# Performance work log

Hardware: AMD Instinct MI355X
Metric: run time of the kernel (lower is better)

The kernel has to match this reference:

```python
import jax, jax.numpy as jnp
import numpy as np

N_NODES = 100000

def gcn_conv(x, edge_index, W, b):
    # torch_geometric GCNConv: add self-loops, sym-normalize, aggregate, add bias
    n = x.shape[0]
    loop = jnp.arange(n)
    src = jnp.concatenate([edge_index[0], loop])  # [E+N]
    dst = jnp.concatenate([edge_index[1], loop])
    h = x @ W  # [N, out]
    deg = jax.ops.segment_sum(jnp.ones_like(dst, dtype=h.dtype), dst, num_segments=n)
    dinv = jnp.where(deg > 0, jax.lax.rsqrt(deg), 0.0)
    norm = dinv[src] * dinv[dst]  # [E+N]
    msg = h[src] * norm[:, None]  # gather + scale
    out = jax.ops.segment_sum(msg, dst, num_segments=n)  # scatter-add
    return out + b

def setup_inputs() -> dict:
    key = jax.random.key(0)
    ks = jax.random.split(key, 6)
    N, F, H, C, E = N_NODES, 128, 128, 32, 1600000
    x = jax.random.normal(ks[0], (N, F), dtype=jnp.float32)
    edge_index = jax.random.randint(ks[1], (2, E), 0, N, dtype=jnp.int64)
    W1 = jax.random.normal(ks[2], (F, H), dtype=jnp.float32) * (1.0 / np.sqrt(F))
    b1 = jnp.zeros((H,), jnp.float32)
    W2 = jax.random.normal(ks[3], (H, H), dtype=jnp.float32) * (1.0 / np.sqrt(H))
    b2 = jnp.zeros((H,), jnp.float32)
    Wc = jax.random.normal(ks[4], (H, C), dtype=jnp.float32) * (1.0 / np.sqrt(H))
    bc = jnp.zeros((C,), jnp.float32)
    return {"x": x, "edge_index": edge_index, "W1": W1, "b1": b1, "W2": W2, "b2": b2, "Wc": Wc, "bc": bc}

def reference(x, edge_index, W1, b1, W2, b2, Wc, bc):
    h = jax.nn.relu(gcn_conv(x, edge_index, W1, b1))
    # dropout is identity in eval mode
    h = jax.nn.relu(gcn_conv(h, edge_index, W2, b2))
    pooled = jnp.mean(h, axis=0)  # [H]
    return pooled @ Wc + bc  # [C]
```

## Files before the change

kernel.cpp:

```cpp
#include <hip/hip_runtime.h>
#include <hip/hip_bf16.h>


#define FEAT 128
#define CHUNK 4096
#define MAXBUCK 512
#define ECAP 12288
#define PBLK 512
#define BPAD 3856

typedef __attribute__((ext_vector_type(8))) short short8;
typedef __attribute__((ext_vector_type(4))) float float4v;
typedef __attribute__((ext_vector_type(2))) float floatx2;

union I4S8 { int4 i; short8 s; };

static __device__ inline unsigned short f2bf(float f) {
    union { __hip_bfloat16 h; unsigned short u; } cv;
    cv.h = __float2bfloat16(f);
    return cv.u;
}

static __device__ inline floatx2 fp8x2_dec(unsigned int u) {
#if __has_builtin(__builtin_amdgcn_cvt_pk_f32_fp8)
    return __builtin_amdgcn_cvt_pk_f32_fp8((int)u, false);
#else
    floatx2 r;
    unsigned int b0 = u & 0xFFu, b1 = (u >> 8) & 0xFFu;
    r.x = __uint_as_float(((b0 & 0x80u) << 24) | ((b0 & 0x7Fu) << 20)) * 0x1p+120f;
    r.y = __uint_as_float(((b1 & 0x80u) << 24) | ((b1 & 0x7Fu) << 20)) * 0x1p+120f;
    return r;
#endif
}

static __device__ inline floatx2 fp8x2_dec_hi(unsigned int u) {
#if __has_builtin(__builtin_amdgcn_cvt_pk_f32_fp8)
    return __builtin_amdgcn_cvt_pk_f32_fp8((int)u, true);
#else
    return fp8x2_dec(u >> 16);
#endif
}

static __device__ inline unsigned short fp8x2_enc(float x, float y) {
#if __has_builtin(__builtin_amdgcn_cvt_pk_fp8_f32)
    return (unsigned short)(__builtin_amdgcn_cvt_pk_fp8_f32(x, y, 0, false) & 0xFFFF);
#else
    auto enc1 = [](float f) -> unsigned int {
        unsigned int u = __float_as_uint(f);
        unsigned int s = (u >> 24) & 0x80u;
        float a = fabsf(f);
        a = fminf(a, 448.0f);
        unsigned int code;
        if (a < 0.015625f) {
            code = (unsigned int)(int)rintf(a * 512.0f);
        } else {
            unsigned int au = __float_as_uint(a);
            unsigned int r = au + 0x0007FFFFu + ((au >> 20) & 1u);
            unsigned int e = (r >> 23) - 120u;
            unsigned int m = (r >> 20) & 7u;
            code = (e << 3) | m;
            if (code > 0x7Eu) code = 0x7Eu;
        }
        return code | s;
    };
    return (unsigned short)(enc1(x) | (enc1(y) << 8));
#endif
}

static __device__ inline unsigned char fp8enc(float f) {
#if __has_builtin(__builtin_amdgcn_cvt_pk_fp8_f32)
    return (unsigned char)(__builtin_amdgcn_cvt_pk_fp8_f32(f, 0.0f, 0, false) & 0xFF);
#else
    return (unsigned char)(fp8x2_enc(f, 0.0f) & 0xFF);
#endif
}

__global__ __launch_bounds__(256) void hist2(const int* __restrict__ dst,
                                             int* __restrict__ hist,
                                             int nE, int NC, int nbuck) {
    __shared__ int h[MAXBUCK];
    int c = blockIdx.x, t = threadIdx.x;
    for (int i = t; i < nbuck; i += 256) h[i] = 0;
    __syncthreads();
    int beg = c * CHUNK, end = min(nE, beg + CHUNK);
    for (int e = beg + t; e < end; e += 256)
        atomicAdd(&h[dst[e] >> 8], 1);
    __syncthreads();
    for (int i = t; i < nbuck; i += 256) hist[i * NC + c] = h[i];
}

__global__ __launch_bounds__(256) void rowsum_k(const int* __restrict__ hist,
                                                int* __restrict__ btot, int NC) {
    __shared__ int red[256];
    int b = blockIdx.x, t = threadIdx.x;
    int s = 0;
    for (int c = t; c < NC; c += 256) s += hist[b * NC + c];
    red[t] = s;
    __syncthreads();
    for (int o = 128; o > 0; o >>= 1) {
        if (t < o) red[t] += red[t + o];
        __syncthreads();
    }
    if (t == 0) btot[b] = red[0];
}

__global__ __launch_bounds__(512) void bscan_k(const int* __restrict__ btot,
                                               int* __restrict__ bboff, int nbuck) {
    __shared__ int sc[512];
    int t = threadIdx.x;
    int v = (t < nbuck) ? btot[t] : 0;
    sc[t] = v;
    __syncthreads();
    for (int o = 1; o < 512; o <<= 1) {
        int add = (t >= o) ? sc[t - o] : 0;
        __syncthreads();
        sc[t] += add;
        __syncthreads();
    }
    if (t < nbuck) {
        bboff[t] = sc[t] - v;
        if (t == nbuck - 1) bboff[nbuck] = sc[t];
    }
}

__global__ __launch_bounds__(512) void rowoff_k(const int* __restrict__ hist,
                                                const int* __restrict__ bboff,
                                                int* __restrict__ hoff, int NC) {
    __shared__ int sc[512];
    int b = blockIdx.x, t = threadIdx.x;
    int v = (t < NC) ? hist[b * NC + t] : 0;
    sc[t] = v;
    __syncthreads();
    for (int o = 1; o < 512; o <<= 1) {
        int add = (t >= o) ? sc[t - o] : 0;
        __syncthreads();
        sc[t] += add;
        __syncthreads();
    }
    if (t < NC) hoff[b * NC + t] = bboff[b] + sc[t] - v;
}

__global__ __launch_bounds__(256) void fill2(const int* __restrict__ src,
                                             const int* __restrict__ dst,
                                             const int* __restrict__ off,
                                             int* __restrict__ binned,
                                             int nE, int NC, int nbuck) {
    __shared__ int cur[MAXBUCK];
    int c = blockIdx.x, t = threadIdx.x;
    for (int i = t; i < nbuck; i += 256) cur[i] = off[i * NC + c];
    __syncthreads();
    int beg = c * CHUNK, end = min(nE, beg + CHUNK);
    for (int e = beg + t; e < end; e += 256) {
        int d = dst[e];
        int pos = atomicAdd(&cur[d >> 8], 1);
        binned[pos] = (src[e] << 8) | (d & 255);
    }
}

__global__ __launch_bounds__(256) void bucket_scat(const int* __restrict__ binned,
                                                   const int* __restrict__ bboff,
                                                   int* __restrict__ cnt,
                                                   float* __restrict__ dinv,
                                                   int* __restrict__ cursor,
                                                   int* __restrict__ csr_src, int n) {
    __shared__ int se[ECAP];
    __shared__ int lcnt[256];
    __shared__ int lcur[256];
    __shared__ int ssc[256];
    int b = blockIdx.x, t = threadIdx.x;
    int node0 = b << 8;
    int nloc = min(256, n - node0);
    int ebeg = bboff[b], eend = bboff[b + 1];
    int ne = eend - ebeg;
    int pbase = (ebeg + b * BPAD + 15) & ~15;
    int zOff = n << 7;
    lcnt[t] = 0;
    __syncthreads();
    bool staged = (ne <= ECAP);
    if (staged) {
        for (int i = t; i < ne; i += 256) {
            int e = binned[ebeg + i];
            se[i] = e;
            atomicAdd(&lcnt[e & 255], 1);
        }
    } else {
        for (int i = t; i < ne; i += 256)
            atomicAdd(&lcnt[binned[ebeg + i] & 255], 1);
    }
    __syncthreads();
    int myc = (t < nloc) ? lcnt[t] : 0;
    int mycp = (myc + 15) & ~15;
    ssc[t] = mycp;
    __syncthreads();
    for (int o = 1; o < 256; o <<= 1) {
        int add = (t >= o) ? ssc[t - o] : 0;
        __syncthreads();
        ssc[t] += add;
        __syncthreads();
    }
    int exclp = ssc[t] - mycp;
    if (t < nloc) {
        cnt[node0 + t] = mycp;
        dinv[node0 + t] = rsqrtf((float)(myc + 1));
        cursor[node0 + t] = pbase + exclp;
        lcur[t] = exclp;
    }
    __syncthreads();
    if (staged) {
        for (int i = t; i < ne; i += 256) {
            int e = se[i];
            int pos = atomicAdd(&lcur[e & 255], 1);
            csr_src[pbase + pos] = (int)(((unsigned int)e >> 8) << 7);
        }
    } else {
        for (int i = t; i < ne; i += 256) {
            int e = binned[ebeg + i];
            int pos = atomicAdd(&lcur[e & 255], 1);
            csr_src[pbase + pos] = (int)(((unsigned int)e >> 8) << 7);
        }
    }
    if (t < nloc) {
        for (int i = exclp + myc; i < exclp + mycp; i++)
            csr_src[pbase + i] = zOff;
    }
}

__global__ __launch_bounds__(256) void wprep2(const float* __restrict__ W1,
                                              const float* __restrict__ W2,
                                              unsigned short* __restrict__ Wbf1,
                                              unsigned short* __restrict__ Wbf2,
                                              unsigned char* __restrict__ gbuf,
                                              int n) {
    int tid = blockIdx.x * 256 + threadIdx.x;
    if (tid < 32)
        ((unsigned int*)(gbuf + (size_t)n * FEAT))[tid] = 0u;
    const float* W = (tid < 16384) ? W1 : W2;
    unsigned short* O = (tid < 16384) ? Wbf1 : Wbf2;
    int id = tid & 16383;
    int chunk = id >> 3, j = id & 7;
    int kb = chunk >> 7, nn = chunk & 127;
    O[id] = f2bf(W[(kb * 8 + j) * FEAT + nn]);
}

template <bool AFP32>
__global__ __launch_bounds__(256) void gemm_mfma(const void* __restrict__ Xv,
                                                 const unsigned short* __restrict__ Wbf,
                                                 const float* __restrict__ dinv,
                                                 unsigned char* __restrict__ gout,
                                                 int n) {
    int wave = threadIdx.x >> 6, lane = threadIdx.x & 63;
    int m0 = blockIdx.x * 64 + wave * 16;
    if (m0 >= n) return;
    int col = lane & 15, quad = lane >> 4;
    int mc = min(m0 + col, n - 1);

    short8 afr[4];
    if (AFP32) {
        const float* X = (const float*)Xv;
        const float* xr = X + (size_t)mc * FEAT + quad * 8;
#pragma unroll
        for (int ks = 0; ks < 4; ks++) {
            float4 lo = *(const float4*)(xr + ks * 32);
            float4 hi = *(const float4*)(xr + ks * 32 + 4);
            short8 a;
            a[0] = (short)f2bf(lo.x); a[1] = (short)f2bf(lo.y);
            a[2] = (short)f2bf(lo.z); a[3] = (short)f2bf(lo.w);
            a[4] = (short)f2bf(hi.x); a[5] = (short)f2bf(hi.y);
            a[6] = (short)f2bf(hi.z); a[7] = (short)f2bf(hi.w);
            afr[ks] = a;
        }
    } else {
        const unsigned char* X8 = (const unsigned char*)Xv;
        const unsigned char* xr = X8 + (size_t)mc * FEAT + quad * 8;
#pragma unroll
        for (int ks = 0; ks < 4; ks++) {
            uint2 u2 = *(const uint2*)(xr + ks * 32);
            floatx2 p0 = fp8x2_dec(u2.x);
            floatx2 p1 = fp8x2_dec_hi(u2.x);
            floatx2 p2 = fp8x2_dec(u2.y);
            floatx2 p3 = fp8x2_dec_hi(u2.y);
            short8 a;
            a[0] = (short)f2bf(p0.x); a[1] = (short)f2bf(p0.y);
            a[2] = (short)f2bf(p1.x); a[3] = (short)f2bf(p1.y);
            a[4] = (short)f2bf(p2.x); a[5] = (short)f2bf(p2.y);
            a[6] = (short)f2bf(p3.x); a[7] = (short)f2bf(p3.y);
            afr[ks] = a;
        }
    }

    float dvr[4];
#pragma unroll
    for (int r = 0; r < 4; r++)
        dvr[r] = dinv[min(m0 + quad * 4 + r, n - 1)];

    const int4* Wb = (const int4*)Wbf;
#pragma unroll
    for (int nt = 0; nt < 8; nt++) {
        float4v acc = {0.f, 0.f, 0.f, 0.f};
#pragma unroll
        for (int ks = 0; ks < 4; ks++) {
            int kb = ks * 4 + quad;
            I4S8 u; u.i = Wb[kb * FEAT + nt * 16 + col];
            acc = __builtin_amdgcn_mfma_f32_16x16x32_bf16(afr[ks], u.s, acc, 0, 0, 0);
        }
#pragma unroll
        for (int r = 0; r < 4; r++) {
            int row = m0 + quad * 4 + r;
            if (row < n)
                gout[(size_t)row * FEAT + nt * 16 + col] = fp8enc(acc[r] * dvr[r]);
        }
    }
}

__global__ __launch_bounds__(256) void agg_csr(const int* __restrict__ cursor,
                                               const int* __restrict__ cnt,
                                               const int* __restrict__ csr_src,
                                               const unsigned char* __restrict__ gbuf,
                                               const float* __restrict__ dinv,
                                               const float* __restrict__ bias,
                                               unsigned short* __restrict__ outb,
                                               int n) {
    int node = blockIdx.x * 4 + (threadIdx.x >> 6);
    if (node >= n) return;
    unsigned lane = threadIdx.x & 63;
    unsigned lane2 = lane << 1;
    int begS = __builtin_amdgcn_readfirstlane(cursor[node]);
    int endS = begS + __builtin_amdgcn_readfirstlane(cnt[node]);
    const unsigned char* csrB = (const unsigned char*)csr_src;

    floatx2 a0 = fp8x2_dec(*(const unsigned short*)(gbuf + ((((unsigned)node) << 7) | lane2)));
    floatx2 a1 = {0.f, 0.f}, a2 = {0.f, 0.f}, a3 = {0.f, 0.f};

    for (int j = begS; j < endS; j += 16) {
        const unsigned char* p = csrB + ((size_t)(unsigned)j << 2);
        int4 w0 = *(const int4*)(p);
        int4 w1 = *(const int4*)(p + 16);
        int4 w2 = *(const int4*)(p + 32);
        int4 w3 = *(const int4*)(p + 48);
        unsigned short uu[16];
        uu[0]  = *(const unsigned short*)(gbuf + ((unsigned)w0.x | lane2));
        uu[1]  = *(const unsigned short*)(gbuf + ((unsigned)w0.y | lane2));
        uu[2]  = *(const unsigned short*)(gbuf + ((unsigned)w0.z | lane2));
        uu[3]  = *(const unsigned short*)(gbuf + ((unsigned)w0.w | lane2));
        uu[4]  = *(const unsigned short*)(gbuf + ((unsigned)w1.x | lane2));
        uu[5]  = *(const unsigned short*)(gbuf + ((unsigned)w1.y | lane2));
        uu[6]  = *(const unsigned short*)(gbuf + ((unsigned)w1.z | lane2));
        uu[7]  = *(const unsigned short*)(gbuf + ((unsigned)w1.w | lane2));
        uu[8]  = *(const unsigned short*)(gbuf + ((unsigned)w2.x | lane2));
        uu[9]  = *(const unsigned short*)(gbuf + ((unsigned)w2.y | lane2));
        uu[10] = *(const unsigned short*)(gbuf + ((unsigned)w2.z | lane2));
        uu[11] = *(const unsigned short*)(gbuf + ((unsigned)w2.w | lane2));
        uu[12] = *(const unsigned short*)(gbuf + ((unsigned)w3.x | lane2));
        uu[13] = *(const unsigned short*)(gbuf + ((unsigned)w3.y | lane2));
        uu[14] = *(const unsigned short*)(gbuf + ((unsigned)w3.z | lane2));
        uu[15] = *(const unsigned short*)(gbuf + ((unsigned)w3.w | lane2));
#pragma unroll
        for (int k = 0; k < 16; k += 4) {
            a0 += fp8x2_dec(uu[k]);
            a1 += fp8x2_dec(uu[k + 1]);
            a2 += fp8x2_dec(uu[k + 2]);
            a3 += fp8x2_dec(uu[k + 3]);
        }
    }
    floatx2 a = (a0 + a1) + (a2 + a3);
    float dv = dinv[node];
    float2 bv = ((const float2*)bias)[lane];
    float rx = fmaxf(a.x * dv + bv.x, 0.0f);
    float ry = fmaxf(a.y * dv + bv.y, 0.0f);
    outb[(((unsigned)node) << 6) | lane] = fp8x2_enc(rx, ry);
}

__global__ __launch_bounds__(256) void pool_kernel(const unsigned char* __restrict__ a,
                                                   float* __restrict__ partial, int n) {
    __shared__ float red[16][132];
    int t = threadIdx.x, b = blockIdx.x;
    int fg = t & 15;
    int rg = t >> 4;
    unsigned fb = (unsigned)fg << 3;
    floatx2 s01 = {0.f, 0.f}, s23 = {0.f, 0.f}, s45 = {0.f, 0.f}, s67 = {0.f, 0.f};
    for (int i = (b << 4) | rg; i < n; i += PBLK * 16) {
        uint2 u2 = *(const uint2*)(a + (((unsigned)i << 7) | fb));
        s01 += fp8x2_dec(u2.x);
        s23 += fp8x2_dec_hi(u2.x);
        s45 += fp8x2_dec(u2.y);
        s67 += fp8x2_dec_hi(u2.y);
    }
    red[rg][fb + 0] = s01.x; red[rg][fb + 1] = s01.y;
    red[rg][fb + 2] = s23.x; red[rg][fb + 3] = s23.y;
    red[rg][fb + 4] = s45.x; red[rg][fb + 5] = s45.y;
    red[rg][fb + 6] = s67.x; red[rg][fb + 7] = s67.y;
    __syncthreads();
    if (t < FEAT) {
        float s = 0.0f;
#pragma unroll
        for (int k = 0; k < 16; k++) s += red[k][t];
        partial[b * FEAT + t] = s;
    }
}

__global__ __launch_bounds__(128) void final_kernel(const float* __restrict__ partial,
                                                    const float* __restrict__ Wc,
                                                    const float* __restrict__ bc,
                                                    float* __restrict__ out,
                                                    int n, int C) {
    __shared__ float p[FEAT];
    int t = threadIdx.x;
    float s = 0.0f;
    for (int b = 0; b < PBLK; b++) s += partial[b * FEAT + t];
    p[t] = s * (1.0f / (float)n);
    __syncthreads();
    if (t < C) {
        float acc = bc[t];
        for (int h = 0; h < FEAT; h++)
            acc += p[h] * Wc[h * C + t];
        out[t] = acc;
    }
}

extern "C" void kernel_launch(void* const* d_in, const int* in_sizes, int n_in,
                              void* d_out, int out_size, void* d_ws, size_t ws_size,
                              hipStream_t stream) {
    const float* x  = (const float*)d_in[0];
    const int*   ei = (const int*)d_in[1];
    const float* W1 = (const float*)d_in[2];
    const float* b1 = (const float*)d_in[3];
    const float* W2 = (const float*)d_in[4];
    const float* b2 = (const float*)d_in[5];
    const float* Wc = (const float*)d_in[6];
    const float* bc = (const float*)d_in[7];

    const int N = in_sizes[0] / FEAT;
    const int E = in_sizes[1] / 2;
    const int C = out_size;
    const int* srcI = ei;
    const int* dstI = ei + E;
    const int NC = (E + CHUNK - 1) / CHUNK;
    const int NBK = (N + 255) >> 8;
    const size_t csrCap = (size_t)E + (size_t)NBK * BPAD + 64;

    auto align256 = [](size_t v) { return (v + 255) & ~(size_t)255; };
    char* w = (char*)d_ws;
    int*            cnt     = (int*)w;            w += align256((size_t)N * 4);
    float*          dinv    = (float*)w;          w += align256((size_t)N * 4);
    int*            cursor  = (int*)w;            w += align256((size_t)N * 4);
    int*            csr_src = (int*)w;            w += align256(csrCap * 4);
    int*            binned  = (int*)w;            w += align256((size_t)E * 4);
    int*            hist    = (int*)w;            w += align256((size_t)NBK * NC * 4);
    int*            hoff    = (int*)w;            w += align256((size_t)NBK * NC * 4);
    int*            btot    = (int*)w;            w += align256((size_t)NBK * 4);
    int*            bboff   = (int*)w;            w += align256((size_t)(NBK + 1) * 4);
    unsigned short* Wbf1    = (unsigned short*)w; w += align256((size_t)FEAT * FEAT * 2);
    unsigned short* Wbf2    = (unsigned short*)w; w += align256((size_t)FEAT * FEAT * 2);
    unsigned char*  gbuf    = (unsigned char*)w;  w += align256((size_t)(N + 1) * FEAT);
    unsigned char*  bufA    = (unsigned char*)w;  w += align256((size_t)N * FEAT);
    float*          partial = (float*)w;          w += align256((size_t)PBLK * FEAT * 4);

    wprep2<<<128, 256, 0, stream>>>(W1, W2, Wbf1, Wbf2, gbuf, N);

    hist2<<<NC, 256, 0, stream>>>(dstI, hist, E, NC, NBK);
    rowsum_k<<<NBK, 256, 0, stream>>>(hist, btot, NC);
    bscan_k<<<1, 512, 0, stream>>>(btot, bboff, NBK);
    rowoff_k<<<NBK, 512, 0, stream>>>(hist, bboff, hoff, NC);
    fill2<<<NC, 256, 0, stream>>>(srcI, dstI, hoff, binned, E, NC, NBK);
    bucket_scat<<<NBK, 256, 0, stream>>>(binned, bboff, cnt, dinv, cursor, csr_src, N);

    const int gGemm = (N + 63) / 64;
    const int gAgg = (N + 3) / 4;

    gemm_mfma<true><<<gGemm, 256, 0, stream>>>(x, Wbf1, dinv, gbuf, N);
    agg_csr<<<gAgg, 256, 0, stream>>>(cursor, cnt, csr_src, gbuf, dinv, b1,
                                      (unsigned short*)bufA, N);

    gemm_mfma<false><<<gGemm, 256, 0, stream>>>(bufA, Wbf2, dinv, gbuf, N);
    agg_csr<<<gAgg, 256, 0, stream>>>(cursor, cnt, csr_src, gbuf, dinv, b2,
                                      (unsigned short*)bufA, N);

    pool_kernel<<<PBLK, 256, 0, stream>>>(bufA, partial, N);
    final_kernel<<<1, 128, 0, stream>>>(partial, Wc, bc, (float*)d_out, N, C);
}
```

Measured before the change: 279.3 us.

## Aggregate two nodes per wavefront with interleaved paired CSR layout

Pairs adjacent destination nodes and interleaves their CSR neighbor lists in 16-entry groups, each pair padded to the larger of the two degrees. The aggregation kernel then gives each half-wavefront one node and has each lane gather 4 fp8 bytes instead of 2, so every wave covers two nodes with wider loads and half as many waves are launched. The cost is extra padding work for pairs whose degrees differ, and BPAD is raised to make room for that larger padded footprint.

```diff
diff --git a/kernel.cpp b/kernel.cpp
--- a/kernel.cpp
+++ b/kernel.cpp
@@ -7,7 +7,7 @@
 #define MAXBUCK 512
 #define ECAP 12288
 #define PBLK 512
-#define BPAD 3856
+#define BPAD 16384
 
 typedef __attribute__((ext_vector_type(8))) short short8;
 typedef __attribute__((ext_vector_type(4))) float float4v;
@@ -167,6 +167,7 @@
     __shared__ int lcnt[256];
     __shared__ int lcur[256];
     __shared__ int ssc[256];
+    __shared__ int poff[128];
     int b = blockIdx.x, t = threadIdx.x;
     int node0 = b << 8;
     int nloc = min(256, n - node0);
@@ -175,6 +176,7 @@
     int pbase = (ebeg + b * BPAD + 15) & ~15;
     int zOff = n << 7;
     lcnt[t] = 0;
+    lcur[t] = 0;
     __syncthreads();
     bool staged = (ne <= ECAP);
     if (staged) {
@@ -189,8 +191,13 @@
     }
     __syncthreads();
     int myc = (t < nloc) ? lcnt[t] : 0;
-    int mycp = (myc + 15) & ~15;
-    ssc[t] = mycp;
+    int npair = (nloc + 1) >> 1;
+    int pairSlots = 0;
+    if (t < npair) {
+        int mx = max(lcnt[2 * t], lcnt[2 * t + 1]);
+        pairSlots = 2 * ((mx + 15) & ~15);
+    }
+    ssc[t] = pairSlots;
     __syncthreads();
     for (int o = 1; o < 256; o <<= 1) {
         int add = (t >= o) ? ssc[t - o] : 0;
@@ -198,30 +205,40 @@
         ssc[t] += add;
         __syncthreads();
     }
-    int exclp = ssc[t] - mycp;
+    if (t < npair) poff[t] = ssc[t] - pairSlots;
+    __syncthreads();
     if (t < nloc) {
-        cnt[node0 + t] = mycp;
+        int p = t >> 1;
+        int pl = ((max(lcnt[p * 2], lcnt[p * 2 + 1]) + 15) & ~15);
+        cnt[node0 + t] = pl;
         dinv[node0 + t] = rsqrtf((float)(myc + 1));
-        cursor[node0 + t] = pbase + exclp;
-        lcur[t] = exclp;
+        cursor[node0 + t] = pbase + poff[p];
     }
     __syncthreads();
     if (staged) {
         for (int i = t; i < ne; i += 256) {
             int e = se[i];
-            int pos = atomicAdd(&lcur[e & 255], 1);
-            csr_src[pbase + pos] = (int)(((unsigned int)e >> 8) << 7);
+            int loc = e & 255;
+            int q = atomicAdd(&lcur[loc], 1);
+            int slot = pbase + poff[loc >> 1] + ((q >> 4) << 5) + ((loc & 1) << 4) + (q & 15);
+            csr_src[slot] = (int)(((unsigned int)e >> 8) << 7);
         }
     } else {
         for (int i = t; i < ne; i += 256) {
             int e = binned[ebeg + i];
-            int pos = atomicAdd(&lcur[e & 255], 1);
-            csr_src[pbase + pos] = (int)(((unsigned int)e >> 8) << 7);
-        }
-    }
-    if (t < nloc) {
-        for (int i = exclp + myc; i < exclp + mycp; i++)
-            csr_src[pbase + i] = zOff;
+            int loc = e & 255;
+            int q = atomicAdd(&lcur[loc], 1);
+            int slot = pbase + poff[loc >> 1] + ((q >> 4) << 5) + ((loc & 1) << 4) + (q & 15);
+            csr_src[slot] = (int)(((unsigned int)e >> 8) << 7);
+        }
+    }
+    int nlocp = (nloc + 1) & ~1;
+    if (t < nlocp) {
+        int p = t >> 1, h = t & 1;
+        int pl = ((max(lcnt[p * 2], lcnt[p * 2 + 1]) + 15) & ~15);
+        int base = pbase + poff[p] + (h << 4);
+        for (int q = myc; q < pl; q++)
+            csr_src[base + ((q >> 4) << 5) + (q & 15)] = zOff;
     }
 }
 
@@ -318,56 +335,68 @@
                                                const unsigned char* __restrict__ gbuf,
                                                const float* __restrict__ dinv,
                                                const float* __restrict__ bias,
-                                               unsigned short* __restrict__ outb,
+                                               unsigned char* __restrict__ outb,
                                                int n) {
-    int node = blockIdx.x * 4 + (threadIdx.x >> 6);
-    if (node >= n) return;
+    int pair = blockIdx.x * 4 + (threadIdx.x >> 6);
+    int nodeA = pair << 1;
+    if (nodeA >= n) return;
     unsigned lane = threadIdx.x & 63;
-    unsigned lane2 = lane << 1;
-    int begS = __builtin_amdgcn_readfirstlane(cursor[node]);
-    int endS = begS + __builtin_amdgcn_readfirstlane(cnt[node]);
+    unsigned half = lane >> 5;
+    unsigned sub = lane & 31;
+    int node = nodeA + (int)half;
+    unsigned fb = sub << 2;
+
+    int curS = __builtin_amdgcn_readfirstlane(cursor[nodeA]);
+    int plS = __builtin_amdgcn_readfirstlane(cnt[nodeA]);
     const unsigned char* csrB = (const unsigned char*)csr_src;
-
-    floatx2 a0 = fp8x2_dec(*(const unsigned short*)(gbuf + ((((unsigned)node) << 7) | lane2)));
-    floatx2 a1 = {0.f, 0.f}, a2 = {0.f, 0.f}, a3 = {0.f, 0.f};
-
-    for (int j = begS; j < endS; j += 16) {
-        const unsigned char* p = csrB + ((size_t)(unsigned)j << 2);
+    const unsigned char* ip0 = csrB + (((size_t)(unsigned)curS) << 2) + (half << 6);
+
+    unsigned su = *(const unsigned*)(gbuf + ((((unsigned)node) << 7) | fb));
+    floatx2 a01 = fp8x2_dec(su), a23 = fp8x2_dec_hi(su);
+    floatx2 b01 = {0.f, 0.f}, b23 = {0.f, 0.f};
+
+    int rounds = plS >> 4;
+    for (int r = 0; r < rounds; r++) {
+        const unsigned char* p = ip0 + ((size_t)(unsigned)r << 7);
         int4 w0 = *(const int4*)(p);
         int4 w1 = *(const int4*)(p + 16);
         int4 w2 = *(const int4*)(p + 32);
         int4 w3 = *(const int4*)(p + 48);
-        unsigned short uu[16];
-        uu[0]  = *(const unsigned short*)(gbuf + ((unsigned)w0.x | lane2));
-        uu[1]  = *(const unsigned short*)(gbuf + ((unsigned)w0.y | lane2));
-        uu[2]  = *(const unsigned short*)(gbuf + ((unsigned)w0.z | lane2));
-        uu[3]  = *(const unsigned short*)(gbuf + ((unsigned)w0.w | lane2));
-        uu[4]  = *(const unsigned short*)(gbuf + ((unsigned)w1.x | lane2));
-        uu[5]  = *(const unsigned short*)(gbuf + ((unsigned)w1.y | lane2));
-        uu[6]  = *(const unsigned short*)(gbuf + ((unsigned)w1.z | lane2));
-        uu[7]  = *(const unsigned short*)(gbuf + ((unsigned)w1.w | lane2));
-        uu[8]  = *(const unsigned short*)(gbuf + ((unsigned)w2.x | lane2));
-        uu[9]  = *(const unsigned short*)(gbuf + ((unsigned)w2.y | lane2));
-        uu[10] = *(const unsigned short*)(gbuf + ((unsigned)w2.z | lane2));
-        uu[11] = *(const unsigned short*)(gbuf + ((unsigned)w2.w | lane2));
-        uu[12] = *(const unsigned short*)(gbuf + ((unsigned)w3.x | lane2));
-        uu[13] = *(const unsigned short*)(gbuf + ((unsigned)w3.y | lane2));
-        uu[14] = *(const unsigned short*)(gbuf + ((unsigned)w3.z | lane2));
-        uu[15] = *(const unsigned short*)(gbuf + ((unsigned)w3.w | lane2));
-#pragma unroll
-        for (int k = 0; k < 16; k += 4) {
-            a0 += fp8x2_dec(uu[k]);
-            a1 += fp8x2_dec(uu[k + 1]);
-            a2 += fp8x2_dec(uu[k + 2]);
-            a3 += fp8x2_dec(uu[k + 3]);
-        }
-    }
-    floatx2 a = (a0 + a1) + (a2 + a3);
+        unsigned uu[16];
+        uu[0]  = *(const unsigned*)(gbuf + ((unsigned)w0.x | fb));
+        uu[1]  = *(const unsigned*)(gbuf + ((unsigned)w0.y | fb));
+        uu[2]  = *(const unsigned*)(gbuf + ((unsigned)w0.z | fb));
+        uu[3]  = *(const unsigned*)(gbuf + ((unsigned)w0.w | fb));
+        uu[4]  = *(const unsigned*)(gbuf + ((unsigned)w1.x | fb));
+        uu[5]  = *(const unsigned*)(gbuf + ((unsigned)w1.y | fb));
+        uu[6]  = *(const unsigned*)(gbuf + ((unsigned)w1.z | fb));
+        uu[7]  = *(const unsigned*)(gbuf + ((unsigned)w1.w | fb));
+        uu[8]  = *(const unsigned*)(gbuf + ((unsigned)w2.x | fb));
+        uu[9]  = *(const unsigned*)(gbuf + ((unsigned)w2.y | fb));
+        uu[10] = *(const unsigned*)(gbuf + ((unsigned)w2.z | fb));
+        uu[11] = *(const unsigned*)(gbuf + ((unsigned)w2.w | fb));
+        uu[12] = *(const unsigned*)(gbuf + ((unsigned)w3.x | fb));
+        uu[13] = *(const unsigned*)(gbuf + ((unsigned)w3.y | fb));
+        uu[14] = *(const unsigned*)(gbuf + ((unsigned)w3.z | fb));
+        uu[15] = *(const unsigned*)(gbuf + ((unsigned)w3.w | fb));
+#pragma unroll
+        for (int k = 0; k < 16; k += 2) {
+            a01 += fp8x2_dec(uu[k]);
+            a23 += fp8x2_dec_hi(uu[k]);
+            b01 += fp8x2_dec(uu[k + 1]);
+            b23 += fp8x2_dec_hi(uu[k + 1]);
+        }
+    }
+    a01 += b01;
+    a23 += b23;
     float dv = dinv[node];
-    float2 bv = ((const float2*)bias)[lane];
-    float rx = fmaxf(a.x * dv + bv.x, 0.0f);
-    float ry = fmaxf(a.y * dv + bv.y, 0.0f);
-    outb[(((unsigned)node) << 6) | lane] = fp8x2_enc(rx, ry);
+    float4 bv = ((const float4*)bias)[sub];
+    float r0 = fmaxf(a01.x * dv + bv.x, 0.0f);
+    float r1 = fmaxf(a01.y * dv + bv.y, 0.0f);
+    float r2 = fmaxf(a23.x * dv + bv.z, 0.0f);
+    float r3 = fmaxf(a23.y * dv + bv.w, 0.0f);
+    unsigned outw = (unsigned)fp8x2_enc(r0, r1) | ((unsigned)fp8x2_enc(r2, r3) << 16);
+    *(unsigned*)(outb + ((((unsigned)node) << 7) | fb)) = outw;
 }
 
 __global__ __launch_bounds__(256) void pool_kernel(const unsigned char* __restrict__ a,
@@ -465,15 +494,15 @@
     bucket_scat<<<NBK, 256, 0, stream>>>(binned, bboff, cnt, dinv, cursor, csr_src, N);
 
     const int gGemm = (N + 63) / 64;
-    const int gAgg = (N + 3) / 4;
+    const int gAgg = (N + 7) / 8;
 
     gemm_mfma<true><<<gGemm, 256, 0, stream>>>(x, Wbf1, dinv, gbuf, N);
     agg_csr<<<gAgg, 256, 0, stream>>>(cursor, cnt, csr_src, gbuf, dinv, b1,
-                                      (unsigned short*)bufA, N);
+                                      bufA, N);
 
     gemm_mfma<false><<<gGemm, 256, 0, stream>>>(bufA, Wbf2, dinv, gbuf, N);
     agg_csr<<<gAgg, 256, 0, stream>>>(cursor, cnt, csr_src, gbuf, dinv, b2,
-                                      (unsigned short*)bufA, N);
+                                      bufA, N);
 
     pool_kernel<<<PBLK, 256, 0, stream>>>(bufA, partial, N);
     final_kernel<<<1, 128, 0, stream>>>(partial, Wc, bc, (float*)d_out, N, C);
```

Result: faster. 266.6 us (median of 2 runs) (-4.6%).
